# Performance work log

Measured on AMD Instinct MI355X. Metric: run time of the kernel, lower is better.

Reference implementation:

```python
import jax, jax.numpy as jnp
import numpy as np

KS = (10, 25, 50, 100)  # numbers of highest-scored tiles to average (eval mode averages over all)
CLAMP = 1e4


def setup_inputs() -> dict:
    key = jax.random.key(0)
    k1, k2, k3, k4, k5, k6, k7 = jax.random.split(key, 7)
    B, C, N, H, O = 8, 2048, 8000, 256, 1000
    x = jax.random.normal(k1, (B, C, N), dtype=jnp.float32)
    # Conv1d(kernel=1) weights == [out, in] matrices
    W0 = jax.random.normal(k2, (H, C), dtype=jnp.float32) * (1.0 / np.sqrt(C))
    b0 = jax.random.normal(k3, (H,), dtype=jnp.float32) * 0.01
    W1 = jax.random.normal(k4, (H, H), dtype=jnp.float32) * (1.0 / np.sqrt(H))
    b1 = jax.random.normal(k5, (H,), dtype=jnp.float32) * 0.01
    W2 = jax.random.normal(k6, (O, H), dtype=jnp.float32) * (1.0 / np.sqrt(H))
    b2 = jax.random.normal(k7, (O,), dtype=jnp.float32) * 0.01
    return {"x": x, "W0": W0, "b0": b0, "W1": W1, "b1": b1, "W2": W2, "b2": b2}


def reference(x, W0, b0, W1, b1, W2, b2):
    # x: [B, C, N] tile features. Eval-mode dropout is identity.
    # mask: tile is 'real' if its max feature > 0 (padding tiles are all-zero)
    mask = (jnp.max(x, axis=1, keepdims=True) > 0).astype(x.dtype)  # [B,1,N]
    # 1x1 conv stack (Conv1d kernel=1 == per-tile matmul)
    h = jnp.einsum('hc,bcn->bhn', W0, x) + b0[None, :, None]
    h = jnp.clip(jax.nn.relu(h), -CLAMP, CLAMP)
    h = jnp.einsum('hg,bgn->bhn', W1, h) + b1[None, :, None]
    h = jnp.clip(jax.nn.relu(h), -CLAMP, CLAMP)
    y = jnp.einsum('oh,bhn->bon', W2, h) + b2[None, :, None]  # [B,O,N]
    y = y * mask
    # top-kmax once (sorted descending); top-k for smaller k is a prefix slice
    kmax = max(KS)
    t, _ = jax.lax.top_k(y, kmax)  # [B,O,kmax]
    pred = jnp.zeros(y.shape[:2], dtype=y.dtype)  # [B,O]
    inv = 1.0 / len(KS)
    for k in KS:
        num = jnp.sum(t[:, :, :k] * mask[:, :, :k], axis=2)  # [B,O]
        den = jnp.sum(mask[:, :, :k], axis=2)                 # [B,1]
        pred = pred + (num / den) * inv
    return pred
```

## Files before the change

### kernel.cpp

```cpp
#include <hip/hip_runtime.h>
#include <hip/hip_bf16.h>
#include <stdint.h>

typedef __bf16 bf16;
typedef __bf16 bf16x8 __attribute__((ext_vector_type(8)));
typedef __bf16 bf16x4 __attribute__((ext_vector_type(4)));
typedef float  floatx4 __attribute__((ext_vector_type(4)));
typedef unsigned int uint32;

#define B_  8
#define C_  2048
#define N_  8000
#define H_  256
#define O_  1000
#define OP_ 1024

__device__ __forceinline__ void gll16(const void* g, void* l) {
  __builtin_amdgcn_global_load_lds((const __attribute__((address_space(1))) void*)g,
                                   (__attribute__((address_space(3))) void*)l, 16, 0, 0);
}

__global__ __launch_bounds__(256) void castw(const float* __restrict__ W0,
                                             const float* __restrict__ W1,
                                             const float* __restrict__ W2,
                                             bf16* __restrict__ W0b,
                                             bf16* __restrict__ W1b,
                                             bf16* __restrict__ W2b) {
  int g = blockIdx.x * 256 + threadIdx.x;
  float4 v;
  bf16* dst;
  if (g < 131072) {
    v = ((const float4*)W0)[g];
    dst = W0b + g * 4;
  } else if (g < 147456) {
    int i = g - 131072;
    v = ((const float4*)W1)[i];
    dst = W1b + i * 4;
  } else {
    int i = g - 147456;
    int o = i >> 6, k4 = i & 63;
    if (o < O_) v = *(const float4*)(W2 + o * 256 + k4 * 4);
    else        v = make_float4(0.f, 0.f, 0.f, 0.f);
    dst = W2b + i * 4;
  }
  bf16x4 r;
  r[0] = (bf16)v.x; r[1] = (bf16)v.y; r[2] = (bf16)v.z; r[3] = (bf16)v.w;
  *(bf16x4*)dst = r;
}

__global__ __launch_bounds__(256) void gemm123(const float* __restrict__ x,
                                               const bf16* __restrict__ W0b,
                                               const float* __restrict__ b0,
                                               const bf16* __restrict__ W1b,
                                               const float* __restrict__ b1,
                                               const bf16* __restrict__ W2b,
                                               const float* __restrict__ b2,
                                               float* __restrict__ maskb,
                                               bf16* __restrict__ yb) {
  __shared__ union {
    struct { bf16 A[256 * 32]; bf16 Bt[64 * 40]; } st;
    bf16 YT[128 * 72];
  } u;
  __shared__ bf16 HT[64 * 264];
  __shared__ float sb[256];
  __shared__ float smk[64];
  __shared__ uint32 nflag[64];

  const int tid  = threadIdx.x;
  const int wave = tid >> 6, lane = tid & 63;
  const int l16  = lane & 15, l4 = lane >> 4;
  const int n0   = blockIdx.x * 64;
  const int b    = blockIdx.y;

  sb[tid] = b0[tid];
  if (tid < 64) nflag[tid] = 0;

  const int kp = tid >> 4;
  const int n4 = (tid & 15) * 4;
  const float* xbase = x + (size_t)b * C_ * N_ + n0 + n4;

  floatx4 acc[4][4];
  #pragma unroll
  for (int i = 0; i < 4; ++i)
    #pragma unroll
    for (int j = 0; j < 4; ++j)
      acc[i][j] = floatx4{0.f, 0.f, 0.f, 0.f};

  uint32 fl = 0;

  for (int k0 = 0; k0 < C_; k0 += 32) {
    #pragma unroll
    for (int i = 0; i < 4; ++i) {
      int c = i * 256 + tid;
      gll16(W0b + (size_t)(c >> 2) * C_ + k0 + (c & 3) * 8, &u.st.A[c * 8]);
    }
    const float* xr = xbase + (size_t)(k0 + 2 * kp) * N_;
    float4 q0 = *(const float4*)xr;
    float4 q1 = *(const float4*)(xr + N_);
    float a0[4] = {q0.x, q0.y, q0.z, q0.w};
    float a1[4] = {q1.x, q1.y, q1.z, q1.w};
    uint32* bw = (uint32*)u.st.Bt;
    #pragma unroll
    for (int i = 0; i < 4; ++i) {
      if (a0[i] > 0.f || a1[i] > 0.f) fl |= (1u << i);
      union { bf16 h[2]; uint32 u32v; } p;
      p.h[0] = (bf16)a0[i];
      p.h[1] = (bf16)a1[i];
      bw[(n4 + i) * 20 + kp] = p.u32v;
    }
    __syncthreads();

    bf16x8 af[4], bfr[4];
    #pragma unroll
    for (int mt = 0; mt < 4; ++mt)
      af[mt] = *(const bf16x8*)&u.st.A[(wave * 64 + mt * 16 + l16) * 32 + l4 * 8];
    #pragma unroll
    for (int nt = 0; nt < 4; ++nt)
      bfr[nt] = *(const bf16x8*)&u.st.Bt[(nt * 16 + l16) * 40 + l4 * 8];
    #pragma unroll
    for (int mt = 0; mt < 4; ++mt)
      #pragma unroll
      for (int nt = 0; nt < 4; ++nt)
        acc[mt][nt] = __builtin_amdgcn_mfma_f32_16x16x32_bf16(af[mt], bfr[nt], acc[mt][nt], 0, 0, 0);
    __syncthreads();
  }

  #pragma unroll
  for (int i = 0; i < 4; ++i)
    if (fl & (1u << i)) atomicOr(&nflag[n4 + i], 1u);
  __syncthreads();
  if (tid < 64) {
    float m = nflag[tid] ? 1.f : 0.f;
    smk[tid] = m;
    maskb[(size_t)b * N_ + n0 + tid] = m;
  }

  #pragma unroll
  for (int mt = 0; mt < 4; ++mt) {
    int m0 = wave * 64 + mt * 16 + l4 * 4;
    #pragma unroll
    for (int nt = 0; nt < 4; ++nt) {
      int n = nt * 16 + l16;
      bf16x4 hv;
      #pragma unroll
      for (int r = 0; r < 4; ++r) {
        float v = acc[mt][nt][r] + sb[m0 + r];
        v = fminf(fmaxf(v, 0.f), 1.0e4f);
        hv[r] = (bf16)v;
      }
      *(bf16x4*)&HT[n * 264 + m0] = hv;
    }
  }
  __syncthreads();

  sb[tid] = b1[tid];
  #pragma unroll
  for (int i = 0; i < 4; ++i)
    #pragma unroll
    for (int j = 0; j < 4; ++j)
      acc[i][j] = floatx4{0.f, 0.f, 0.f, 0.f};

  for (int k0 = 0; k0 < 256; k0 += 32) {
    #pragma unroll
    for (int i = 0; i < 4; ++i) {
      int c = i * 256 + tid;
      gll16(W1b + (size_t)(c >> 2) * 256 + k0 + (c & 3) * 8, &u.st.A[c * 8]);
    }
    __syncthreads();

    bf16x8 af[4], bfr[4];
    #pragma unroll
    for (int mt = 0; mt < 4; ++mt)
      af[mt] = *(const bf16x8*)&u.st.A[(wave * 64 + mt * 16 + l16) * 32 + l4 * 8];
    #pragma unroll
    for (int nt = 0; nt < 4; ++nt)
      bfr[nt] = *(const bf16x8*)&HT[(nt * 16 + l16) * 264 + k0 + l4 * 8];
    #pragma unroll
    for (int mt = 0; mt < 4; ++mt)
      #pragma unroll
      for (int nt = 0; nt < 4; ++nt)
        acc[mt][nt] = __builtin_amdgcn_mfma_f32_16x16x32_bf16(af[mt], bfr[nt], acc[mt][nt], 0, 0, 0);
    __syncthreads();
  }

  #pragma unroll
  for (int mt = 0; mt < 4; ++mt) {
    int m0 = wave * 64 + mt * 16 + l4 * 4;
    #pragma unroll
    for (int nt = 0; nt < 4; ++nt) {
      int n = nt * 16 + l16;
      bf16x4 hv;
      #pragma unroll
      for (int r = 0; r < 4; ++r) {
        float v = acc[mt][nt][r] + sb[m0 + r];
        v = fminf(fmaxf(v, 0.f), 1.0e4f);
        hv[r] = (bf16)v;
      }
      *(bf16x4*)&HT[n * 264 + m0] = hv;
    }
  }
  __syncthreads();

  for (int mb = 0; mb < 4; ++mb) {
    const int m0g = mb * 256;
    { int og = m0g + tid; sb[tid] = (og < O_) ? b2[og] : 0.f; }

    #pragma unroll
    for (int i = 0; i < 4; ++i)
      #pragma unroll
      for (int j = 0; j < 4; ++j)
        acc[i][j] = floatx4{0.f, 0.f, 0.f, 0.f};

    for (int k0 = 0; k0 < 256; k0 += 32) {
      #pragma unroll
      for (int i = 0; i < 4; ++i) {
        int c = i * 256 + tid;
        gll16(W2b + (size_t)(m0g + (c >> 2)) * 256 + k0 + (c & 3) * 8, &u.st.A[c * 8]);
      }
      __syncthreads();

      bf16x8 af[4], bfr[4];
      #pragma unroll
      for (int mt = 0; mt < 4; ++mt)
        af[mt] = *(const bf16x8*)&u.st.A[(wave * 64 + mt * 16 + l16) * 32 + l4 * 8];
      #pragma unroll
      for (int nt = 0; nt < 4; ++nt)
        bfr[nt] = *(const bf16x8*)&HT[(nt * 16 + l16) * 264 + k0 + l4 * 8];
      #pragma unroll
      for (int mt = 0; mt < 4; ++mt)
        #pragma unroll
        for (int nt = 0; nt < 4; ++nt)
          acc[mt][nt] = __builtin_amdgcn_mfma_f32_16x16x32_bf16(af[mt], bfr[nt], acc[mt][nt], 0, 0, 0);
      __syncthreads();
    }

    #pragma unroll
    for (int h = 0; h < 2; ++h) {
      #pragma unroll
      for (int mt = 0; mt < 4; ++mt) {
        int m0 = wave * 64 + mt * 16 + l4 * 4;
        if ((m0 >> 7) == h) {
          #pragma unroll
          for (int nt = 0; nt < 4; ++nt) {
            int n = nt * 16 + l16;
            float m = smk[n];
            #pragma unroll
            for (int r = 0; r < 4; ++r)
              u.YT[(m0 - h * 128 + r) * 72 + n] = (bf16)((acc[mt][nt][r] + sb[m0 + r]) * m);
          }
        }
      }
      __syncthreads();
      {
        int row = tid >> 1, ch = tid & 1;
        int og = m0g + h * 128 + row;
        if (og < O_) {
          const char* src = (const char*)&u.YT[row * 72 + ch * 32];
          bf16* dst = yb + ((size_t)b * OP_ + og) * N_ + n0 + ch * 32;
          #pragma unroll
          for (int j = 0; j < 4; ++j)
            *(uint4*)((char*)dst + j * 16) = *(const uint4*)(src + j * 16);
        }
      }
      __syncthreads();
    }
  }
}

__global__ __launch_bounds__(64) void topk(const bf16* __restrict__ y,
                                           const float* __restrict__ maskb,
                                           float* __restrict__ out) {
  __shared__ uint32 cand[128];
  __shared__ float  sval[128];
  __shared__ float  m100[100];
  __shared__ int    gcnt;

  const int lane = threadIdx.x;
  const int o = blockIdx.x, b = blockIdx.y;

  const uint32* yw = (const uint32*)(y + ((size_t)b * OP_ + o) * N_);
  const float*  mr = maskb + (size_t)b * N_;

  if (lane == 0) gcnt = 0;
  m100[lane] = mr[lane];
  if (lane < 36) m100[64 + lane] = mr[64 + lane];

  uint32 khi[64];
  #pragma unroll
  for (int i = 0; i < 16; ++i) {
    int base = i * 256 + lane * 4;
    bool real = (base < 4000);
    uint4 v = make_uint4(0u, 0u, 0u, 0u);
    if (real) v = *(const uint4*)(yw + base);
    uint32 ww[4] = {v.x, v.y, v.z, v.w};
    #pragma unroll
    for (int j = 0; j < 4; ++j) {
      uint32 w = ww[j];
      uint32 sgn = w & 0x80008000u;
      uint32 mskk = 0x80008000u | (sgn - (sgn >> 15));
      uint32 k = w ^ mskk;
      if (!real) k = 0u;
      khi[i * 4 + j] = k;
    }
  }

  uint32 prefix = 0;
  #pragma unroll 1
  for (int bit = 15; bit >= 0; --bit) {
    uint32 T16 = (prefix | (1u << bit)) << 16;
    int c = 0;
    #pragma unroll
    for (int r = 0; r < 64; ++r) {
      c += (khi[r] >= T16);
      c += ((khi[r] << 16) >= T16);
    }
    #pragma unroll
    for (int m = 1; m < 64; m <<= 1) c += __shfl_xor(c, m, 64);
    if (c >= 100) prefix |= (1u << bit);
  }

  #pragma unroll
  for (int r = 0; r < 64; ++r) {
    uint32 h = khi[r] >> 16;
    uint32 l = khi[r] & 0xffffu;
    if (h > prefix) { int p = atomicAdd(&gcnt, 1); cand[p] = h; }
    if (l > prefix) { int p = atomicAdd(&gcnt, 1); cand[p] = l; }
  }
  __syncthreads();
  int cg = gcnt;
  for (int idx = lane; idx < 100; idx += 64)
    if (idx >= cg) cand[idx] = prefix;
  __syncthreads();

  for (int idx = lane; idx < 100; idx += 64) {
    uint32 ci = cand[idx];
    int rank = 0;
    for (int j = 0; j < 100; ++j) {
      uint32 cj = cand[j];
      rank += (cj > ci) || (cj == ci && j < idx);
    }
    uint32 bb = (ci & 0x8000u) ? (ci & 0x7fffu) : (~ci & 0xffffu);
    sval[rank] = __uint_as_float(bb << 16);
  }
  __syncthreads();

  if (lane == 0) {
    const int KSv[4] = {10, 25, 50, 100};
    float num = 0.f, den = 0.f, pred = 0.f;
    int ki = 0;
    for (int j = 0; j < 100; ++j) {
      num += sval[j] * m100[j];
      den += m100[j];
      if (j + 1 == KSv[ki]) { pred += 0.25f * num / den; ++ki; }
    }
    out[(size_t)b * O_ + o] = pred;
  }
}

extern "C" void kernel_launch(void* const* d_in, const int* in_sizes, int n_in,
                              void* d_out, int out_size, void* d_ws, size_t ws_size,
                              hipStream_t stream) {
  const float* x  = (const float*)d_in[0];
  const float* W0 = (const float*)d_in[1];
  const float* b0 = (const float*)d_in[2];
  const float* W1 = (const float*)d_in[3];
  const float* b1 = (const float*)d_in[4];
  const float* W2 = (const float*)d_in[5];
  const float* b2 = (const float*)d_in[6];
  float* out = (float*)d_out;

  char* ws = (char*)d_ws;
  bf16*  W0b  = (bf16*)(ws + 0);
  bf16*  W1b  = (bf16*)(ws + 1048576);
  bf16*  W2b  = (bf16*)(ws + 1179648);
  float* mk   = (float*)(ws + 1703936);
  bf16*  yb   = (bf16*)(ws + 1959936);

  castw<<<832, 256, 0, stream>>>(W0, W1, W2, W0b, W1b, W2b);
  gemm123<<<dim3(125, 8), 256, 0, stream>>>(x, W0b, b0, W1b, b1, W2b, b2, mk, yb);
  topk<<<dim3(1000, 8), 64, 0, stream>>>(yb, mk, out);
}
```

Baseline: 923.0 us.

## Double-buffer LDS tiles in all three GEMM loops with one barrier per step

Splits the A and Bt staging buffers into two halves so that the next K-slice's weight tile (global_load_lds) and x rows are fetched while MFMAs run on the current slice. The fetch is hoisted into a prologue, and waits use raw s_waitcnt plus s_barrier, cutting each loop from two barriers per iteration to one. The aim is to hide global-load latency in the large C=2048 first GEMM and in the small W1/W2 GEMMs. The cost is roughly doubled staging LDS, which may lower the number of resident blocks per CU.

New measurement: 916.2 us. About the same (-0.7%).

```diff
diff --git a/kernel.cpp b/kernel.cpp
--- a/kernel.cpp
+++ b/kernel.cpp
@@ -19,6 +19,9 @@
   __builtin_amdgcn_global_load_lds((const __attribute__((address_space(1))) void*)g,
                                    (__attribute__((address_space(3))) void*)l, 16, 0, 0);
 }
+__device__ __forceinline__ void wait_vm0()   { asm volatile("s_waitcnt vmcnt(0)" ::: "memory"); }
+__device__ __forceinline__ void wait_lgkm0() { asm volatile("s_waitcnt lgkmcnt(0)" ::: "memory"); }
+__device__ __forceinline__ void bar_raw()    { __builtin_amdgcn_s_barrier(); }
 
 __global__ __launch_bounds__(256) void castw(const float* __restrict__ W0,
                                              const float* __restrict__ W1,
@@ -58,7 +61,7 @@
                                                float* __restrict__ maskb,
                                                bf16* __restrict__ yb) {
   __shared__ union {
-    struct { bf16 A[256 * 32]; bf16 Bt[64 * 40]; } st;
+    struct { bf16 A[2][256 * 32]; bf16 Bt[2][64 * 40]; } st;
     bf16 YT[128 * 72];
   } u;
   __shared__ bf16 HT[64 * 264];
@@ -88,41 +91,54 @@
 
   uint32 fl = 0;
 
+  #pragma unroll
+  for (int i = 0; i < 4; ++i) {
+    int c = i * 256 + tid;
+    gll16(W0b + (size_t)(c >> 2) * C_ + (c & 3) * 8, &u.st.A[0][c * 8]);
+  }
+  float4 q0 = *(const float4*)(xbase + (size_t)(2 * kp) * N_);
+  float4 q1 = *(const float4*)(xbase + (size_t)(2 * kp + 1) * N_);
+
   for (int k0 = 0; k0 < C_; k0 += 32) {
-    #pragma unroll
-    for (int i = 0; i < 4; ++i) {
-      int c = i * 256 + tid;
-      gll16(W0b + (size_t)(c >> 2) * C_ + k0 + (c & 3) * 8, &u.st.A[c * 8]);
-    }
-    const float* xr = xbase + (size_t)(k0 + 2 * kp) * N_;
-    float4 q0 = *(const float4*)xr;
-    float4 q1 = *(const float4*)(xr + N_);
-    float a0[4] = {q0.x, q0.y, q0.z, q0.w};
-    float a1[4] = {q1.x, q1.y, q1.z, q1.w};
-    uint32* bw = (uint32*)u.st.Bt;
-    #pragma unroll
-    for (int i = 0; i < 4; ++i) {
-      if (a0[i] > 0.f || a1[i] > 0.f) fl |= (1u << i);
-      union { bf16 h[2]; uint32 u32v; } p;
-      p.h[0] = (bf16)a0[i];
-      p.h[1] = (bf16)a1[i];
-      bw[(n4 + i) * 20 + kp] = p.u32v;
-    }
-    __syncthreads();
-
+    const int cur = (k0 >> 5) & 1, nxt = cur ^ 1;
+    wait_vm0();
+    {
+      float a0[4] = {q0.x, q0.y, q0.z, q0.w};
+      float a1[4] = {q1.x, q1.y, q1.z, q1.w};
+      uint32* bw = (uint32*)u.st.Bt[cur];
+      #pragma unroll
+      for (int i = 0; i < 4; ++i) {
+        if (a0[i] > 0.f || a1[i] > 0.f) fl |= (1u << i);
+        union { bf16 h[2]; uint32 u32v; } p;
+        p.h[0] = (bf16)a0[i];
+        p.h[1] = (bf16)a1[i];
+        bw[(n4 + i) * 20 + kp] = p.u32v;
+      }
+    }
+    wait_lgkm0();
+    bar_raw();
+    if (k0 + 32 < C_) {
+      #pragma unroll
+      for (int i = 0; i < 4; ++i) {
+        int c = i * 256 + tid;
+        gll16(W0b + (size_t)(c >> 2) * C_ + (k0 + 32) + (c & 3) * 8, &u.st.A[nxt][c * 8]);
+      }
+      const float* xr = xbase + (size_t)(k0 + 32 + 2 * kp) * N_;
+      q0 = *(const float4*)xr;
+      q1 = *(const float4*)(xr + N_);
+    }
     bf16x8 af[4], bfr[4];
     #pragma unroll
     for (int mt = 0; mt < 4; ++mt)
-      af[mt] = *(const bf16x8*)&u.st.A[(wave * 64 + mt * 16 + l16) * 32 + l4 * 8];
+      af[mt] = *(const bf16x8*)&u.st.A[cur][(wave * 64 + mt * 16 + l16) * 32 + l4 * 8];
     #pragma unroll
     for (int nt = 0; nt < 4; ++nt)
-      bfr[nt] = *(const bf16x8*)&u.st.Bt[(nt * 16 + l16) * 40 + l4 * 8];
+      bfr[nt] = *(const bf16x8*)&u.st.Bt[cur][(nt * 16 + l16) * 40 + l4 * 8];
     #pragma unroll
     for (int mt = 0; mt < 4; ++mt)
       #pragma unroll
       for (int nt = 0; nt < 4; ++nt)
         acc[mt][nt] = __builtin_amdgcn_mfma_f32_16x16x32_bf16(af[mt], bfr[nt], acc[mt][nt], 0, 0, 0);
-    __syncthreads();
   }
 
   #pragma unroll
@@ -160,18 +176,26 @@
     for (int j = 0; j < 4; ++j)
       acc[i][j] = floatx4{0.f, 0.f, 0.f, 0.f};
 
+  #pragma unroll
+  for (int i = 0; i < 4; ++i) {
+    int c = i * 256 + tid;
+    gll16(W1b + (size_t)(c >> 2) * 256 + (c & 3) * 8, &u.st.A[0][c * 8]);
+  }
   for (int k0 = 0; k0 < 256; k0 += 32) {
-    #pragma unroll
-    for (int i = 0; i < 4; ++i) {
-      int c = i * 256 + tid;
-      gll16(W1b + (size_t)(c >> 2) * 256 + k0 + (c & 3) * 8, &u.st.A[c * 8]);
-    }
-    __syncthreads();
-
+    const int cur = (k0 >> 5) & 1, nxt = cur ^ 1;
+    wait_vm0();
+    bar_raw();
+    if (k0 + 32 < 256) {
+      #pragma unroll
+      for (int i = 0; i < 4; ++i) {
+        int c = i * 256 + tid;
+        gll16(W1b + (size_t)(c >> 2) * 256 + (k0 + 32) + (c & 3) * 8, &u.st.A[nxt][c * 8]);
+      }
+    }
     bf16x8 af[4], bfr[4];
     #pragma unroll
     for (int mt = 0; mt < 4; ++mt)
-      af[mt] = *(const bf16x8*)&u.st.A[(wave * 64 + mt * 16 + l16) * 32 + l4 * 8];
+      af[mt] = *(const bf16x8*)&u.st.A[cur][(wave * 64 + mt * 16 + l16) * 32 + l4 * 8];
     #pragma unroll
     for (int nt = 0; nt < 4; ++nt)
       bfr[nt] = *(const bf16x8*)&HT[(nt * 16 + l16) * 264 + k0 + l4 * 8];
@@ -180,8 +204,8 @@
       #pragma unroll
       for (int nt = 0; nt < 4; ++nt)
         acc[mt][nt] = __builtin_amdgcn_mfma_f32_16x16x32_bf16(af[mt], bfr[nt], acc[mt][nt], 0, 0, 0);
-    __syncthreads();
-  }
+  }
+  __syncthreads();
 
   #pragma unroll
   for (int mt = 0; mt < 4; ++mt) {
@@ -211,18 +235,26 @@
       for (int j = 0; j < 4; ++j)
         acc[i][j] = floatx4{0.f, 0.f, 0.f, 0.f};
 
+    #pragma unroll
+    for (int i = 0; i < 4; ++i) {
+      int c = i * 256 + tid;
+      gll16(W2b + (size_t)(m0g + (c >> 2)) * 256 + (c & 3) * 8, &u.st.A[0][c * 8]);
+    }
     for (int k0 = 0; k0 < 256; k0 += 32) {
-      #pragma unroll
-      for (int i = 0; i < 4; ++i) {
-        int c = i * 256 + tid;
-        gll16(W2b + (size_t)(m0g + (c >> 2)) * 256 + k0 + (c & 3) * 8, &u.st.A[c * 8]);
-      }
-      __syncthreads();
-
+      const int cur = (k0 >> 5) & 1, nxt = cur ^ 1;
+      wait_vm0();
+      bar_raw();
+      if (k0 + 32 < 256) {
+        #pragma unroll
+        for (int i = 0; i < 4; ++i) {
+          int c = i * 256 + tid;
+          gll16(W2b + (size_t)(m0g + (c >> 2)) * 256 + (k0 + 32) + (c & 3) * 8, &u.st.A[nxt][c * 8]);
+        }
+      }
       bf16x8 af[4], bfr[4];
       #pragma unroll
       for (int mt = 0; mt < 4; ++mt)
-        af[mt] = *(const bf16x8*)&u.st.A[(wave * 64 + mt * 16 + l16) * 32 + l4 * 8];
+        af[mt] = *(const bf16x8*)&u.st.A[cur][(wave * 64 + mt * 16 + l16) * 32 + l4 * 8];
       #pragma unroll
       for (int nt = 0; nt < 4; ++nt)
         bfr[nt] = *(const bf16x8*)&HT[(nt * 16 + l16) * 264 + k0 + l4 * 8];
@@ -231,8 +263,8 @@
         #pragma unroll
         for (int nt = 0; nt < 4; ++nt)
           acc[mt][nt] = __builtin_amdgcn_mfma_f32_16x16x32_bf16(af[mt], bfr[nt], acc[mt][nt], 0, 0, 0);
-      __syncthreads();
-    }
+    }
+    __syncthreads();
 
     #pragma unroll
     for (int h = 0; h < 2; ++h) {
```
